# Optimization experiments

Measured on AMD Instinct MI355X. Metric: run time of the kernel, lower is better.

Reference implementation:

```python
import jax, jax.numpy as jnp
import numpy as np
import math

B, S, D, H, DK = 4, 2048, 1024, 8, 128  # d_k = d_v = D // H

def setup_inputs() -> dict:
    key = jax.random.key(0)
    ks = jax.random.split(key, 7)
    scale = 0.02
    x = jax.random.normal(ks[0], (B, S, D), dtype=jnp.float32)
    mask = jax.random.randint(ks[1], (B, S), 0, 2, dtype=jnp.int32)
    W_q = jax.random.normal(ks[2], (H, D, DK), dtype=jnp.float32) * scale
    W_k = jax.random.normal(ks[3], (H, D, DK), dtype=jnp.float32) * scale
    W_v = jax.random.normal(ks[4], (H, D, DK), dtype=jnp.float32) * scale
    W_o = jax.random.normal(ks[5], (D, H * DK), dtype=jnp.float32) * scale
    bias = jnp.zeros((1,), dtype=jnp.float32)
    return {"x": x, "mask": mask, "W_q": W_q, "W_k": W_k, "W_v": W_v, "W_o": W_o, "bias": bias}

def reference(x, mask, W_q, W_k, W_v, W_o, bias):
    # Batched form of the per-head loop: Q/K/V share a scalar bias.
    b = bias[0]
    Q = jnp.einsum('bsd,hdk->bhsk', x, W_q) + b
    K = jnp.einsum('bsd,hdk->bhsk', x, W_k) + b
    V = jnp.einsum('bsd,hdk->bhsk', x, W_v) + b
    scale = 1.0 / math.sqrt(DK)
    scores = jnp.einsum('bhsk,bhtk->bhst', Q, K) * scale  # [B,H,S,S]
    m = mask[:, None, None, :].astype(scores.dtype)  # key mask [B,1,1,S]
    scores = scores + (1.0 - m) * (-1e30)  # masked_softmax
    p = jax.nn.softmax(scores, axis=-1)
    heads = jnp.einsum('bhst,bhtv->bhsv', p, V)  # [B,H,S,DK]
    # torch.cat prepends each new head => heads concatenated in reverse order
    heads = heads[:, ::-1]
    multihead = heads.transpose(0, 2, 1, 3).reshape(B, S, H * DK)
    out = multihead @ W_o.T + b  # dropout is identity in eval mode
    return out
```

## Files before the change

### kernel.cpp

```cpp
#include <hip/hip_runtime.h>
#include <math.h>


typedef __bf16 bf16;
typedef __bf16 bf16x2 __attribute__((ext_vector_type(2)));
typedef __bf16 bf16x4 __attribute__((ext_vector_type(4)));
typedef __bf16 bf16x8 __attribute__((ext_vector_type(8)));
typedef float  f32x4  __attribute__((ext_vector_type(4)));
typedef float  f32x16 __attribute__((ext_vector_type(16)));
typedef int    i32x4  __attribute__((ext_vector_type(4)));

constexpr float QK_SCALE = 0.08838834764831845f;

__device__ __forceinline__ void load16_to_lds(const bf16* g, bf16* l) {
    __builtin_amdgcn_global_load_lds((const __attribute__((address_space(1))) void*)g,
                                     (__attribute__((address_space(3))) void*)l,
                                     16, 0, 0);
}

__device__ __forceinline__ int packbf2(float a, float b) {
    bf16x2 v; v[0] = (bf16)a; v[1] = (bf16)b;
    return __builtin_bit_cast(int, v);
}

template <int CMODE>
__global__ __launch_bounds__(256, 2)
void gemm_nt(const bf16* __restrict__ A, const bf16* __restrict__ Bm,
             void* __restrict__ Cv, bf16* __restrict__ vT,
             const float* __restrict__ bias, const int* __restrict__ gmask,
             int K, int lda, int ldb, int ldc)
{
    __shared__ alignas(16) bf16 As[128 * 32];
    __shared__ alignas(16) bf16 Bs[128 * 32];

    const int m0 = blockIdx.x * 128;
    const int n0 = blockIdx.y * 128;
    const int t    = threadIdx.x;
    const int lane = t & 63;
    const int wv   = t >> 6;
    const int mw   = (wv >> 1) * 64;
    const int nw   = (wv & 1) * 64;

    const int r1 = t >> 2;
    const int c1 = ((t & 3) - (r1 >> 1)) & 3;
    const int r2 = r1 + 64;
    const int c2 = ((t & 3) - (r2 >> 1)) & 3;

    const bf16* ga1 = A  + (long)(m0 + r1) * lda + c1 * 8;
    const bf16* ga2 = A  + (long)(m0 + r2) * lda + c2 * 8;
    const bf16* gb1 = Bm + (long)(n0 + r1) * ldb + c1 * 8;
    const bf16* gb2 = Bm + (long)(n0 + r2) * ldb + c2 * 8;
    bf16* la1 = &As[t * 8];
    bf16* la2 = &As[(256 + t) * 8];
    bf16* lb1 = &Bs[t * 8];
    bf16* lb2 = &Bs[(256 + t) * 8];

    const int fr = lane & 15;
    const int fq = lane >> 4;
    int aoff[4], boff[4];
#pragma unroll
    for (int i = 0; i < 4; ++i) {
        int Ra = mw + i * 16 + fr;
        aoff[i] = (Ra * 4 + ((fq + (Ra >> 1)) & 3)) * 8;
        int Rb = nw + i * 16 + fr;
        boff[i] = (Rb * 4 + ((fq + (Rb >> 1)) & 3)) * 8;
    }

    const f32x4 zero4 = {0.f, 0.f, 0.f, 0.f};
    f32x4 acc[4][4];
#pragma unroll
    for (int i = 0; i < 4; ++i)
#pragma unroll
        for (int j = 0; j < 4; ++j) acc[i][j] = zero4;

    for (int k0 = 0; k0 < K; k0 += 32) {
        __syncthreads();
        load16_to_lds(ga1, la1);
        load16_to_lds(ga2, la2);
        load16_to_lds(gb1, lb1);
        load16_to_lds(gb2, lb2);
        ga1 += 32; ga2 += 32; gb1 += 32; gb2 += 32;
        __syncthreads();
        bf16x8 af[4], bfr[4];
#pragma unroll
        for (int i = 0; i < 4; ++i) af[i]  = *(const bf16x8*)&As[aoff[i]];
#pragma unroll
        for (int j = 0; j < 4; ++j) bfr[j] = *(const bf16x8*)&Bs[boff[j]];
#pragma unroll
        for (int i = 0; i < 4; ++i)
#pragma unroll
            for (int j = 0; j < 4; ++j)
                acc[i][j] = __builtin_amdgcn_mfma_f32_16x16x32_bf16(af[i], bfr[j], acc[i][j], 0, 0, 0);
    }

    float bval = 0.f;
    if (CMODE == 1 || CMODE == 2) bval = bias[0];

#pragma unroll
    for (int i = 0; i < 4; ++i) {
        const int row0 = m0 + mw + i * 16 + fq * 4;
#pragma unroll
        for (int j = 0; j < 4; ++j) {
            const int col = n0 + nw + j * 16 + fr;
            if (CMODE == 2) {
                float* C = (float*)Cv;
#pragma unroll
                for (int r = 0; r < 4; ++r)
                    C[(long)(row0 + r) * ldc + col] = acc[i][j][r] + bval;
            } else {
                bf16* C = (bf16*)Cv;
                if (col < 2048) {
                    const float badd = (col < 1024) ? bval * QK_SCALE : bval;
#pragma unroll
                    for (int r = 0; r < 4; ++r)
                        C[(long)(row0 + r) * ldc + col] = (bf16)(acc[i][j][r] + badd);
                } else {
                    const int vcol = col - 2048;
                    const int h  = vcol >> 7;
                    const int dk = vcol & 127;
                    const int b  = row0 >> 11;
                    const int s  = row0 & 2047;
                    i32x4 m4 = *(const i32x4*)(gmask + b * 2048 + s);
                    bf16x4 pack;
#pragma unroll
                    for (int r = 0; r < 4; ++r)
                        pack[r] = (bf16)((acc[i][j][r] + bval) * (float)m4[r]);
                    *(bf16x4*)&vT[((long)((b * 8 + h) * 128 + dk)) * 2048 + s] = pack;
                }
            }
        }
    }
}

__global__ __launch_bounds__(256, 2)
void flash2(const bf16* __restrict__ qk, const bf16* __restrict__ vT,
            const bf16* __restrict__ mbf, bf16* __restrict__ mh)
{
    __shared__ alignas(16) bf16 Kh[128 * 128];
    __shared__ alignas(16) bf16 Vh[128 * 128];

    const int qt = blockIdx.x, bh = blockIdx.y;
    const int b = bh >> 3, h = bh & 7;
    const int q0 = qt * 128;
    const int t = threadIdx.x, lane = t & 63, wv = t >> 6;
    const int l31 = lane & 31;
    const int hl  = lane >> 5;

    const bf16* Qb = qk + ((long)(b * 2048 + q0)) * 2048 + h * 128;
    const bf16* Kb = qk + (long)b * 2048 * 2048 + 1024 + h * 128;
    const bf16* Vb = vT + (long)bh * 128 * 2048;
    const bf16* mrow = mbf + b * 2048;

    const int r0 = t >> 4;
    const int co = (((t & 15) - r0) & 15) * 8;
    bf16* ldK = &Kh[t * 8];
    bf16* ldV = &Vh[t * 8];

    {
        const bf16* s = Qb + (long)r0 * 2048 + co;
#pragma unroll
        for (int rnd = 0; rnd < 8; ++rnd)
            load16_to_lds(s + (long)rnd * 16 * 2048, ldK + rnd * 2048);
    }
    __syncthreads();
    bf16x8 qf[8];
#pragma unroll
    for (int kc = 0; kc < 8; ++kc) {
        int row = wv * 32 + l31;
        int pos = ((kc * 2 + hl) + row) & 15;
        qf[kc] = *(const bf16x8*)&Kh[row * 128 + pos * 8];
    }
    __syncthreads();

    {
        const bf16* sk = Kb + (long)r0 * 2048 + co;
        const bf16* sv = Vb + (long)r0 * 2048 + co;
#pragma unroll
        for (int rnd = 0; rnd < 8; ++rnd) {
            load16_to_lds(sk + (long)rnd * 16 * 2048, ldK + rnd * 2048);
            load16_to_lds(sv + (long)rnd * 16 * 2048, ldV + rnd * 2048);
        }
    }
    __syncthreads();

    f32x16 O4[4], lac;
#pragma unroll
    for (int r = 0; r < 16; ++r) {
        lac[r] = 0.f;
#pragma unroll
        for (int nt = 0; nt < 4; ++nt) O4[nt][r] = 0.f;
    }

    for (int t0 = 0; t0 < 2048; t0 += 128) {
        bf16x8 pf[8];
#pragma unroll
        for (int mt = 0; mt < 4; ++mt) {
            f32x16 S;
#pragma unroll
            for (int r = 0; r < 16; ++r) S[r] = 0.f;
#pragma unroll
            for (int kc = 0; kc < 8; ++kc) {
                int row = mt * 32 + l31;
                int pos = ((kc * 2 + hl) + row) & 15;
                bf16x8 kf = *(const bf16x8*)&Kh[row * 128 + pos * 8];
                S = __builtin_amdgcn_mfma_f32_32x32x16_bf16(kf, qf[kc], S, 0, 0, 0);
            }
            int ownd[4][2];
#pragma unroll
            for (int g = 0; g < 4; ++g) {
                float e0 = __expf(S[g * 4 + 0]);
                float e1 = __expf(S[g * 4 + 1]);
                float e2 = __expf(S[g * 4 + 2]);
                float e3 = __expf(S[g * 4 + 3]);
                ownd[g][0] = packbf2(e0, e1);
                ownd[g][1] = packbf2(e2, e3);
            }
            int rcv[4][2];
#pragma unroll
            for (int g = 0; g < 4; ++g) {
                rcv[g][0] = __shfl_xor(ownd[g][0], 32);
                rcv[g][1] = __shfl_xor(ownd[g][1], 32);
            }
#pragma unroll
            for (int kk = 0; kk < 2; ++kk) {
                i32x4 w;
                w[0] = hl ? rcv[2 * kk + 1][0] : ownd[2 * kk][0];
                w[1] = hl ? rcv[2 * kk + 1][1] : ownd[2 * kk][1];
                w[2] = hl ? ownd[2 * kk + 1][0] : rcv[2 * kk][0];
                w[3] = hl ? ownd[2 * kk + 1][1] : rcv[2 * kk][1];
                pf[mt * 2 + kk] = __builtin_bit_cast(bf16x8, w);
            }
        }

        __syncthreads();

        bf16x8 mf[8];
#pragma unroll
        for (int kc = 0; kc < 8; ++kc)
            mf[kc] = *(const bf16x8*)(mrow + t0 + kc * 16 + hl * 8);

        if (t0 < 2048 - 128) {
            const bf16* sk = Kb + (long)(t0 + 128 + r0) * 2048 + co;
#pragma unroll
            for (int rnd = 0; rnd < 8; ++rnd)
                load16_to_lds(sk + (long)rnd * 16 * 2048, ldK + rnd * 2048);
        }

#pragma unroll
        for (int kc = 0; kc < 8; ++kc)
            lac = __builtin_amdgcn_mfma_f32_32x32x16_bf16(pf[kc], mf[kc], lac, 0, 0, 0);

#pragma unroll
        for (int kc = 0; kc < 8; ++kc) {
#pragma unroll
            for (int nt = 0; nt < 4; ++nt) {
                int row = nt * 32 + l31;
                int pos = ((kc * 2 + hl) + row) & 15;
                bf16x8 vf = *(const bf16x8*)&Vh[row * 128 + pos * 8];
                O4[nt] = __builtin_amdgcn_mfma_f32_32x32x16_bf16(pf[kc], vf, O4[nt], 0, 0, 0);
            }
        }

        __syncthreads();

        if (t0 < 2048 - 128) {
            const bf16* sv = Vb + (long)r0 * 2048 + (t0 + 128) + co;
#pragma unroll
            for (int rnd = 0; rnd < 8; ++rnd)
                load16_to_lds(sv + (long)rnd * 16 * 2048, ldV + rnd * 2048);
        }
    }

    float invl[16];
#pragma unroll
    for (int r = 0; r < 16; ++r) invl[r] = 1.0f / lac[r];
    bf16* outb = mh + ((long)(b * 2048 + q0 + wv * 32)) * 1024 + (7 - h) * 128;
#pragma unroll
    for (int nt = 0; nt < 4; ++nt)
#pragma unroll
        for (int r = 0; r < 16; ++r) {
            int row = (r & 3) + 8 * (r >> 2) + 4 * hl;
            outb[(long)row * 1024 + nt * 32 + l31] = (bf16)(O4[nt][r] * invl[r]);
        }
}

__global__ __launch_bounds__(256)
void pack_f32_bf16(const float* __restrict__ src, bf16* __restrict__ dst, int n)
{
    int i = (blockIdx.x * 256 + threadIdx.x) * 4;
    if (i >= n) return;
    float4 f = *(const float4*)(src + i);
    bf16x4 o;
    o[0] = (bf16)f.x; o[1] = (bf16)f.y; o[2] = (bf16)f.z; o[3] = (bf16)f.w;
    *(bf16x4*)(dst + i) = o;
}

__global__ __launch_bounds__(256)
void pack_mask(const int* __restrict__ mask, bf16* __restrict__ mbf, int n)
{
    int i = (blockIdx.x * 256 + threadIdx.x) * 4;
    if (i >= n) return;
    i32x4 m = *(const i32x4*)(mask + i);
    bf16x4 o;
#pragma unroll
    for (int r = 0; r < 4; ++r) o[r] = (bf16)(float)m[r];
    *(bf16x4*)(mbf + i) = o;
}

__global__ __launch_bounds__(256)
void pack_wt(const float* __restrict__ Wq, const float* __restrict__ Wk,
             const float* __restrict__ Wv, bf16* __restrict__ wt)
{
    __shared__ float tile[64][65];
    const int which = blockIdx.z;
    const float* W = (which == 0) ? Wq : (which == 1) ? Wk : Wv;
    const float scale = (which == 0) ? QK_SCALE : 1.0f;
    const int h  = blockIdx.y;
    const int d0 = (blockIdx.x >> 1) * 64;
    const int k0 = (blockIdx.x & 1) * 64;
    const float* Wh = W + (long)h * 1024 * 128;
#pragma unroll
    for (int it = 0; it < 16; ++it) {
        int e = it * 256 + threadIdx.x;
        int r = e >> 6, c = e & 63;
        tile[r][c] = Wh[(long)(d0 + r) * 128 + (k0 + c)];
    }
    __syncthreads();
#pragma unroll
    for (int it = 0; it < 16; ++it) {
        int e = it * 256 + threadIdx.x;
        int rk = e >> 6, cd = e & 63;
        int n = which * 1024 + h * 128 + k0 + rk;
        wt[(long)n * 1024 + d0 + cd] = (bf16)(tile[cd][rk] * scale);
    }
}

extern "C" void kernel_launch(void* const* d_in, const int* in_sizes, int n_in,
                              void* d_out, int out_size, void* d_ws, size_t ws_size,
                              hipStream_t stream)
{
    const float* x    = (const float*)d_in[0];
    const int*   mask = (const int*)d_in[1];
    const float* Wq   = (const float*)d_in[2];
    const float* Wk   = (const float*)d_in[3];
    const float* Wv   = (const float*)d_in[4];
    const float* Wo   = (const float*)d_in[5];
    const float* bias = (const float*)d_in[6];
    float* out = (float*)d_out;

    char* w = (char*)d_ws;
    bf16* xb  = (bf16*)w; w += (size_t)8192 * 1024 * 2;
    bf16* wt  = (bf16*)w; w += (size_t)3072 * 1024 * 2;
    bf16* wob = (bf16*)w; w += (size_t)1024 * 1024 * 2;
    bf16* qk  = (bf16*)w; w += (size_t)8192 * 2048 * 2;
    bf16* vT  = (bf16*)w; w += (size_t)32 * 128 * 2048 * 2;
    bf16* mh  = (bf16*)w; w += (size_t)8192 * 1024 * 2;
    bf16* mbf = (bf16*)w; w += (size_t)4 * 2048 * 2;

    pack_f32_bf16<<<8192, 256, 0, stream>>>(x, xb, 8192 * 1024);
    pack_f32_bf16<<<1024, 256, 0, stream>>>(Wo, wob, 1024 * 1024);
    pack_mask<<<8, 256, 0, stream>>>(mask, mbf, 8192);
    pack_wt<<<dim3(32, 8, 3), 256, 0, stream>>>(Wq, Wk, Wv, wt);

    gemm_nt<1><<<dim3(64, 24), 256, 0, stream>>>(
        xb, wt, qk, vT, bias, mask, 1024, 1024, 1024, 2048);

    flash2<<<dim3(16, 32), 256, 0, stream>>>(qk, vT, mbf, mh);

    gemm_nt<2><<<dim3(64, 8), 256, 0, stream>>>(
        mh, wob, out, nullptr, bias, nullptr, 1024, 1024, 1024, 1024);
}
```

Baseline: 273.8 us.

## Double-buffer K in LDS, read V from global, widen flash blocks

The attention kernel becomes 512 threads covering 256 query rows per block. K tiles are now double-buffered in LDS, so the next tile's load overlaps the current tile's compute, which removes one barrier per iteration. V fragments and mask values are read straight from global memory instead of being staged through LDS. The three small packing kernels are merged into a single launch. Reading V from global relies on cache hits and can stall the MFMA chain, and the larger block halves the grid to 256 blocks.

```diff
diff --git a/kernel.cpp b/kernel.cpp
--- a/kernel.cpp
+++ b/kernel.cpp
@@ -132,16 +132,16 @@
     }
 }
 
-__global__ __launch_bounds__(256, 2)
-void flash2(const bf16* __restrict__ qk, const bf16* __restrict__ vT,
+__global__ __launch_bounds__(512, 2)
+void flash3(const bf16* __restrict__ qk, const bf16* __restrict__ vT,
             const bf16* __restrict__ mbf, bf16* __restrict__ mh)
 {
-    __shared__ alignas(16) bf16 Kh[128 * 128];
-    __shared__ alignas(16) bf16 Vh[128 * 128];
+    __shared__ alignas(16) bf16 KbufA[128 * 128];
+    __shared__ alignas(16) bf16 KbufB[128 * 128];
 
     const int qt = blockIdx.x, bh = blockIdx.y;
     const int b = bh >> 3, h = bh & 7;
-    const int q0 = qt * 128;
+    const int q0 = qt * 256;
     const int t = threadIdx.x, lane = t & 63, wv = t >> 6;
     const int l31 = lane & 31;
     const int hl  = lane >> 5;
@@ -153,35 +153,31 @@
 
     const int r0 = t >> 4;
     const int co = (((t & 15) - r0) & 15) * 8;
-    bf16* ldK = &Kh[t * 8];
-    bf16* ldV = &Vh[t * 8];
-
-    {
-        const bf16* s = Qb + (long)r0 * 2048 + co;
-#pragma unroll
-        for (int rnd = 0; rnd < 8; ++rnd)
-            load16_to_lds(s + (long)rnd * 16 * 2048, ldK + rnd * 2048);
-    }
+    bf16* ldA = &KbufA[t * 8];
+    bf16* ldB = &KbufB[t * 8];
+
+#pragma unroll
+    for (int rnd = 0; rnd < 4; ++rnd)
+        load16_to_lds(Qb + (long)(rnd * 32 + r0) * 2048 + co, ldA + rnd * 4096);
+#pragma unroll
+    for (int rnd = 0; rnd < 4; ++rnd)
+        load16_to_lds(Qb + (long)((rnd + 4) * 32 + r0) * 2048 + co, ldB + rnd * 4096);
     __syncthreads();
     bf16x8 qf[8];
-#pragma unroll
-    for (int kc = 0; kc < 8; ++kc) {
-        int row = wv * 32 + l31;
-        int pos = ((kc * 2 + hl) + row) & 15;
-        qf[kc] = *(const bf16x8*)&Kh[row * 128 + pos * 8];
+    {
+        const bf16* qsrc = (wv < 4) ? KbufA : KbufB;
+        const int rloc = (wv & 3) * 32 + l31;
+#pragma unroll
+        for (int kc = 0; kc < 8; ++kc) {
+            int pos = ((kc * 2 + hl) + rloc) & 15;
+            qf[kc] = *(const bf16x8*)&qsrc[rloc * 128 + pos * 8];
+        }
     }
     __syncthreads();
 
-    {
-        const bf16* sk = Kb + (long)r0 * 2048 + co;
-        const bf16* sv = Vb + (long)r0 * 2048 + co;
-#pragma unroll
-        for (int rnd = 0; rnd < 8; ++rnd) {
-            load16_to_lds(sk + (long)rnd * 16 * 2048, ldK + rnd * 2048);
-            load16_to_lds(sv + (long)rnd * 16 * 2048, ldV + rnd * 2048);
-        }
-    }
-    __syncthreads();
+#pragma unroll
+    for (int rnd = 0; rnd < 4; ++rnd)
+        load16_to_lds(Kb + (long)(rnd * 32 + r0) * 2048 + co, ldA + rnd * 4096);
 
     f32x16 O4[4], lac;
 #pragma unroll
@@ -191,7 +187,19 @@
         for (int nt = 0; nt < 4; ++nt) O4[nt][r] = 0.f;
     }
 
-    for (int t0 = 0; t0 < 2048; t0 += 128) {
+    for (int tt = 0; tt < 16; ++tt) {
+        const int t0 = tt * 128;
+        __syncthreads();
+
+        if (tt < 15) {
+            bf16* ld = (tt & 1) ? ldA : ldB;
+            const bf16* src = Kb + (long)(t0 + 128 + r0) * 2048 + co;
+#pragma unroll
+            for (int rnd = 0; rnd < 4; ++rnd)
+                load16_to_lds(src + (long)rnd * 32 * 2048, ld + rnd * 4096);
+        }
+        const bf16* KH = (tt & 1) ? KbufB : KbufA;
+
         bf16x8 pf[8];
 #pragma unroll
         for (int mt = 0; mt < 4; ++mt) {
@@ -202,7 +210,7 @@
             for (int kc = 0; kc < 8; ++kc) {
                 int row = mt * 32 + l31;
                 int pos = ((kc * 2 + hl) + row) & 15;
-                bf16x8 kf = *(const bf16x8*)&Kh[row * 128 + pos * 8];
+                bf16x8 kf = *(const bf16x8*)&KH[row * 128 + pos * 8];
                 S = __builtin_amdgcn_mfma_f32_32x32x16_bf16(kf, qf[kc], S, 0, 0, 0);
             }
             int ownd[4][2];
@@ -232,42 +240,20 @@
             }
         }
 
-        __syncthreads();
-
-        bf16x8 mf[8];
-#pragma unroll
-        for (int kc = 0; kc < 8; ++kc)
-            mf[kc] = *(const bf16x8*)(mrow + t0 + kc * 16 + hl * 8);
-
-        if (t0 < 2048 - 128) {
-            const bf16* sk = Kb + (long)(t0 + 128 + r0) * 2048 + co;
-#pragma unroll
-            for (int rnd = 0; rnd < 8; ++rnd)
-                load16_to_lds(sk + (long)rnd * 16 * 2048, ldK + rnd * 2048);
-        }
-
-#pragma unroll
-        for (int kc = 0; kc < 8; ++kc)
-            lac = __builtin_amdgcn_mfma_f32_32x32x16_bf16(pf[kc], mf[kc], lac, 0, 0, 0);
-
 #pragma unroll
         for (int kc = 0; kc < 8; ++kc) {
+            bf16x8 mf = *(const bf16x8*)(mrow + t0 + kc * 16 + hl * 8);
+            lac = __builtin_amdgcn_mfma_f32_32x32x16_bf16(pf[kc], mf, lac, 0, 0, 0);
+        }
+
+#pragma unroll
+        for (int kc = 0; kc < 8; ++kc) {
 #pragma unroll
             for (int nt = 0; nt < 4; ++nt) {
-                int row = nt * 32 + l31;
-                int pos = ((kc * 2 + hl) + row) & 15;
-                bf16x8 vf = *(const bf16x8*)&Vh[row * 128 + pos * 8];
+                bf16x8 vf = *(const bf16x8*)(Vb + (long)(nt * 32 + l31) * 2048
+                                             + t0 + kc * 16 + hl * 8);
                 O4[nt] = __builtin_amdgcn_mfma_f32_32x32x16_bf16(pf[kc], vf, O4[nt], 0, 0, 0);
             }
-        }
-
-        __syncthreads();
-
-        if (t0 < 2048 - 128) {
-            const bf16* sv = Vb + (long)r0 * 2048 + (t0 + 128) + co;
-#pragma unroll
-            for (int rnd = 0; rnd < 8; ++rnd)
-                load16_to_lds(sv + (long)rnd * 16 * 2048, ldV + rnd * 2048);
         }
     }
 
@@ -285,26 +271,33 @@
 }
 
 __global__ __launch_bounds__(256)
-void pack_f32_bf16(const float* __restrict__ src, bf16* __restrict__ dst, int n)
-{
-    int i = (blockIdx.x * 256 + threadIdx.x) * 4;
-    if (i >= n) return;
-    float4 f = *(const float4*)(src + i);
-    bf16x4 o;
-    o[0] = (bf16)f.x; o[1] = (bf16)f.y; o[2] = (bf16)f.z; o[3] = (bf16)f.w;
-    *(bf16x4*)(dst + i) = o;
-}
-
-__global__ __launch_bounds__(256)
-void pack_mask(const int* __restrict__ mask, bf16* __restrict__ mbf, int n)
-{
-    int i = (blockIdx.x * 256 + threadIdx.x) * 4;
-    if (i >= n) return;
-    i32x4 m = *(const i32x4*)(mask + i);
-    bf16x4 o;
-#pragma unroll
-    for (int r = 0; r < 4; ++r) o[r] = (bf16)(float)m[r];
-    *(bf16x4*)(mbf + i) = o;
+void pack_all(const float* __restrict__ x, const float* __restrict__ Wo,
+              const int* __restrict__ mask,
+              bf16* __restrict__ xb, bf16* __restrict__ wob, bf16* __restrict__ mbf)
+{
+    const long n1 = 8192L * 1024, n2 = 1024L * 1024;
+    long i = ((long)blockIdx.x * 256 + threadIdx.x) * 4;
+    if (i < n1) {
+        float4 f = *(const float4*)(x + i);
+        bf16x4 o;
+        o[0] = (bf16)f.x; o[1] = (bf16)f.y; o[2] = (bf16)f.z; o[3] = (bf16)f.w;
+        *(bf16x4*)(xb + i) = o;
+    } else if (i < n1 + n2) {
+        long j = i - n1;
+        float4 f = *(const float4*)(Wo + j);
+        bf16x4 o;
+        o[0] = (bf16)f.x; o[1] = (bf16)f.y; o[2] = (bf16)f.z; o[3] = (bf16)f.w;
+        *(bf16x4*)(wob + j) = o;
+    } else {
+        long j = i - n1 - n2;
+        if (j < 8192) {
+            i32x4 m = *(const i32x4*)(mask + j);
+            bf16x4 o;
+#pragma unroll
+            for (int r = 0; r < 4; ++r) o[r] = (bf16)(float)m[r];
+            *(bf16x4*)(mbf + j) = o;
+        }
+    }
 }
 
 __global__ __launch_bounds__(256)
@@ -357,15 +350,13 @@
     bf16* mh  = (bf16*)w; w += (size_t)8192 * 1024 * 2;
     bf16* mbf = (bf16*)w; w += (size_t)4 * 2048 * 2;
 
-    pack_f32_bf16<<<8192, 256, 0, stream>>>(x, xb, 8192 * 1024);
-    pack_f32_bf16<<<1024, 256, 0, stream>>>(Wo, wob, 1024 * 1024);
-    pack_mask<<<8, 256, 0, stream>>>(mask, mbf, 8192);
+    pack_all<<<9224, 256, 0, stream>>>(x, Wo, mask, xb, wob, mbf);
     pack_wt<<<dim3(32, 8, 3), 256, 0, stream>>>(Wq, Wk, Wv, wt);
 
     gemm_nt<1><<<dim3(64, 24), 256, 0, stream>>>(
         xb, wt, qk, vT, bias, mask, 1024, 1024, 1024, 2048);
 
-    flash2<<<dim3(16, 32), 256, 0, stream>>>(qk, vT, mbf, mh);
+    flash3<<<dim3(8, 32), 512, 0, stream>>>(qk, vT, mbf, mh);
 
     gemm_nt<2><<<dim3(64, 8), 256, 0, stream>>>(
         mh, wob, out, nullptr, bias, nullptr, 1024, 1024, 1024, 1024);
```

Result: slower. 362.7 us (+32.5%).
